# Performance work log

Hardware: AMD Instinct MI355X
Metric: run time of the kernel (lower is better)

Reference implementation:

```python
import jax, jax.numpy as jnp
import numpy as np

B, S = 2, 2048          # 2 sequences of length 2048 (prefill, equal-length varlen batch)
H, HKV, D = 32, 1, 64   # query heads, kv heads (MQA), head size
HID = H * D             # 2048
T = B * S
SCALE = D ** -0.5


def setup_inputs() -> dict:
    key = jax.random.key(0)
    k1, k2, k3 = jax.random.split(key, 3)
    hidden_states = jax.random.normal(k1, (T, HID), dtype=jnp.float32)
    # rotary tables: positions restart per sequence, NeoX half-rotation, base 10000
    inv_freq = 1.0 / (10000.0 ** (jnp.arange(0, D, 2, dtype=jnp.float32) / D))  # [D/2]
    pos = jnp.tile(jnp.arange(S, dtype=jnp.float32), B)                          # [T]
    freqs = pos[:, None] * inv_freq[None, :]                                     # [T, D/2]
    cos = jnp.cos(freqs)[:, None, :]                                             # [T,1,D/2]
    sin = jnp.sin(freqs)[:, None, :]
    w_qkv = jax.random.normal(k2, ((H + 2 * HKV) * D, HID), dtype=jnp.float32) * (HID ** -0.5)
    w_dense = jax.random.normal(k3, (HID, H * D), dtype=jnp.float32) * (HID ** -0.5)
    return {"hidden_states": hidden_states, "cos": cos, "sin": sin,
            "w_qkv": w_qkv, "w_dense": w_dense}


def _rope(x, cos, sin):
    # x: [T, nh, D]; cos/sin: [T, 1, D/2]; NeoX-style half rotation
    x1, x2 = x[..., : D // 2], x[..., D // 2:]
    return jnp.concatenate([x1 * cos - x2 * sin, x2 * cos + x1 * sin], axis=-1)


def reference(hidden_states, cos, sin, w_qkv, w_dense):
    qkv = hidden_states @ w_qkv.T                                # [T, (H+2*HKV)*D]
    q, kvf = jnp.split(qkv, [H * D], axis=1)
    q = q.reshape(T, H, D)
    kv = kvf.reshape(T, 2, HKV, D)
    q = _rope(q, cos, sin)
    k = _rope(kv[:, 0], cos, sin)                                # [T, HKV, D]
    v = kv[:, 1]                                                 # [T, HKV, D]
    # varlen prefill attention: reshape to [B,S,...]; MQA broadcast kv over H heads
    qb = q.reshape(B, S, H, D)
    kb = k.reshape(B, S, HKV, D)[:, :, 0, :]                     # [B,S,D]
    vb = v.reshape(B, S, HKV, D)[:, :, 0, :]
    scores = jnp.einsum("bshd,btd->bhst", qb, kb) * SCALE        # [B,H,S,S]
    causal = jnp.tril(jnp.ones((S, S), dtype=bool))
    scores = jnp.where(causal[None, None], scores, jnp.float32(-1e30))
    probs = jax.nn.softmax(scores, axis=-1)
    attn = jnp.einsum("bhst,btd->bshd", probs, vb)               # [B,S,H,D]
    return attn.reshape(T, H * D) @ w_dense.T                    # [T, HID]
```

## Files before the change

### kernel.cpp

```cpp
#include <hip/hip_runtime.h>

#define BB   2
#define SS   2048
#define TT   4096
#define HH   32
#define DD   64
#define HIDN 2048
#define NQKV 2176
#define QK_SCALE_LOG2 0.1803368801f

#define AS1 __attribute__((address_space(1)))
#define AS3 __attribute__((address_space(3)))

typedef __attribute__((ext_vector_type(8))) short short8;
typedef __attribute__((ext_vector_type(4))) float f32x4;
typedef __attribute__((ext_vector_type(16))) float f32x16;
typedef __attribute__((ext_vector_type(4))) unsigned short ushort4_t;
typedef __attribute__((ext_vector_type(4))) unsigned int uint4_t;

__device__ inline unsigned short f2bf(float f) {
  unsigned int u = __builtin_bit_cast(unsigned int, f);
  u += 0x7FFFu + ((u >> 16) & 1u);
  return (unsigned short)(u >> 16);
}
__device__ inline float bf2f(unsigned short s) {
  unsigned int u = ((unsigned int)s) << 16;
  return __builtin_bit_cast(float, u);
}
__device__ inline float exp2fast(float x) { return __builtin_amdgcn_exp2f(x); }

__global__ __launch_bounds__(256)
void cvt_kernel(const float* __restrict__ in, unsigned short* __restrict__ out, int n4) {
  int i = blockIdx.x * 256 + threadIdx.x;
  if (i >= n4) return;
  float4 v = ((const float4*)in)[i];
  ushort4_t u = { f2bf(v.x), f2bf(v.y), f2bf(v.z), f2bf(v.w) };
  *(ushort4_t*)(out + (long)i * 4) = u;
}

template<int OUT_BF16>
__global__ __launch_bounds__(256)
void gemm_bt(const unsigned short* __restrict__ A, const unsigned short* __restrict__ Bw,
             void* __restrict__ Cp, int M, int N, int K) {
  __shared__ unsigned char lAB[32768];
  const int tid  = threadIdx.x;
  const int lane = tid & 63;
  const int wv   = tid >> 6;
  const int wr   = wv >> 1, wc = wv & 1;
  const int g    = lane >> 4, qq = lane & 15;
  const long bm0 = (long)blockIdx.y * 128;
  const long bn0 = (long)blockIdx.x * 128;
  const int srow  = tid >> 3;
  const int scolu = ((((tid & 7) << 4) ^ ((srow & 7) << 4)) >> 1);

  f32x4 zero = {0.f, 0.f, 0.f, 0.f};
  f32x4 acc[4][4];
#pragma unroll
  for (int m = 0; m < 4; ++m)
#pragma unroll
    for (int n = 0; n < 4; ++n) acc[m][n] = zero;

  const unsigned short* aSrc = A  + (bm0 + srow) * K + scolu;
  const unsigned short* bSrc = Bw + (bn0 + srow) * K + scolu;
  const int rswz = (qq & 7) << 4;

  for (int k0 = 0; k0 < K; k0 += 64) {
    __syncthreads();
#pragma unroll
    for (int gg = 0; gg < 4; ++gg) {
      __builtin_amdgcn_global_load_lds(
          (const AS1 unsigned int*)(aSrc + k0 + (long)32 * gg * K),
          (AS3 unsigned int*)(lAB + gg * 4096 + wv * 1024), 16, 0, 0);
      __builtin_amdgcn_global_load_lds(
          (const AS1 unsigned int*)(bSrc + k0 + (long)32 * gg * K),
          (AS3 unsigned int*)(lAB + 16384 + gg * 4096 + wv * 1024), 16, 0, 0);
    }
    __syncthreads();

#pragma unroll
    for (int ks = 0; ks < 2; ++ks) {
      short8 af[4], bf[4];
#pragma unroll
      for (int m = 0; m < 4; ++m)
        af[m] = *(const short8*)(lAB + (wr * 64 + m * 16 + qq) * 128
                                     + ((ks * 64 + g * 16) ^ rswz));
#pragma unroll
      for (int n = 0; n < 4; ++n)
        bf[n] = *(const short8*)(lAB + 16384 + (wc * 64 + n * 16 + qq) * 128
                                     + ((ks * 64 + g * 16) ^ rswz));
#pragma unroll
      for (int m = 0; m < 4; ++m)
#pragma unroll
        for (int n = 0; n < 4; ++n)
          acc[m][n] = __builtin_amdgcn_mfma_f32_16x16x32_bf16(af[m], bf[n], acc[m][n], 0, 0, 0);
    }
  }

#pragma unroll
  for (int m = 0; m < 4; ++m) {
#pragma unroll
    for (int r = 0; r < 4; ++r) {
      long row = bm0 + wr * 64 + m * 16 + g * 4 + r;
#pragma unroll
      for (int n = 0; n < 4; ++n) {
        long col = bn0 + wc * 64 + n * 16 + qq;
        float v = acc[m][n][r];
        if (OUT_BF16) ((unsigned short*)Cp)[row * N + col] = f2bf(v);
        else          ((float*)Cp)[row * N + col] = v;
      }
    }
  }
}

__global__ __launch_bounds__(256)
void rope_kernel(const unsigned short* __restrict__ qkv, const float* __restrict__ cosb,
                 const float* __restrict__ sinb, unsigned short* __restrict__ q_out,
                 unsigned short* __restrict__ k_out, unsigned short* __restrict__ v_out) {
  int idx = blockIdx.x * 256 + threadIdx.x;
  if (idx >= TT * 136) return;
  int t   = idx / 136;
  int rem = idx - t * 136;
  int hh  = rem >> 2;
  int i0  = (rem & 3) * 8;
  const unsigned short* row = qkv + (long)t * NQKV;

  if (hh < 33) {
    const unsigned short* src = row + (hh < 32 ? hh * 64 : 2048);
    short8 a = *(const short8*)(src + i0);
    short8 b = *(const short8*)(src + 32 + i0);
    float cv[8], sv[8];
    *(float4*)(cv)     = *(const float4*)(cosb + t * 32 + i0);
    *(float4*)(cv + 4) = *(const float4*)(cosb + t * 32 + i0 + 4);
    *(float4*)(sv)     = *(const float4*)(sinb + t * 32 + i0);
    *(float4*)(sv + 4) = *(const float4*)(sinb + t * 32 + i0 + 4);
    const float sc = (hh < 32) ? QK_SCALE_LOG2 : 1.f;
    short8 ra, rb;
#pragma unroll
    for (int j = 0; j < 8; ++j) {
      float x1 = bf2f((unsigned short)a[j]);
      float x2 = bf2f((unsigned short)b[j]);
      ra[j] = (short)f2bf((x1 * cv[j] - x2 * sv[j]) * sc);
      rb[j] = (short)f2bf((x2 * cv[j] + x1 * sv[j]) * sc);
    }
    unsigned short* dst = (hh < 32) ? q_out + ((long)t * 32 + hh) * 64
                                    : k_out + (long)t * 64;
    *(short8*)(dst + i0)      = ra;
    *(short8*)(dst + 32 + i0) = rb;
  } else {
    const unsigned short* src = row + 2112;
    short8 a = *(const short8*)(src + i0);
    short8 b = *(const short8*)(src + 32 + i0);
    int bb = t >> 11, s = t & 2047;
    int tile = s >> 6, c = s & 63;
    long base = ((long)bb * 32 + tile) * 64;
#pragma unroll
    for (int j = 0; j < 8; ++j) {
      v_out[(base + i0 + j) * 64 + c]      = (unsigned short)a[j];
      v_out[(base + 32 + i0 + j) * 64 + c] = (unsigned short)b[j];
    }
  }
}

__global__ __launch_bounds__(256, 2)
void attn_kernel(const unsigned short* __restrict__ qs, const unsigned short* __restrict__ kr,
                 const unsigned short* __restrict__ vt, unsigned short* __restrict__ ob) {
  __shared__ unsigned char lsm[32768];
  const int tid  = threadIdx.x;
  const int lane = tid & 63;
  const int wv   = tid >> 6;
  const int half = lane >> 5;
  const int qc   = lane & 31;
  const int h    = blockIdx.y * 4 + wv;
  const int b    = blockIdx.z;
  const int qtA  = blockIdx.x;
  const int qtB  = (SS / 32 - 1) - blockIdx.x;
  const int q0A  = qtA * 32, q0B = qtB * 32;
  const int nbA  = (q0A >> 7) + 1, nbB = (q0B >> 7) + 1;

  const unsigned short* kb  = kr + (long)b * SS * 64;
  const unsigned short* vtb = vt + (long)b * (SS / 64) * 64 * 64;

  const int srow = tid >> 3;
  const int scol = ((((tid & 7) << 4) ^ ((srow & 7) << 4)) >> 1);

  const int rswz = (qc & 7) << 4;
  int roff[4];
#pragma unroll
  for (int i = 0; i < 4; ++i)
    roff[i] = qc * 128 + ((i * 32 + half * 16) ^ rswz);

  short8 qfA[4], qfB[4];
  {
    const unsigned short* qrA = qs + ((long)(b * SS + q0A + qc) * HH + h) * 64;
    const unsigned short* qrB = qs + ((long)(b * SS + q0B + qc) * HH + h) * 64;
#pragma unroll
    for (int dstep = 0; dstep < 4; ++dstep) {
      qfA[dstep] = *(const short8*)(qrA + dstep * 16 + half * 8);
      qfB[dstep] = *(const short8*)(qrB + dstep * 16 + half * 8);
    }
  }

  f32x16 oA0, oA1, oB0, oB1;
#pragma unroll
  for (int r = 0; r < 16; ++r) { oA0[r] = 0.f; oA1[r] = 0.f; oB0[r] = 0.f; oB1[r] = 0.f; }
  float mA = -1e30f, lA = 0.f, mB = -1e30f, lB = 0.f;

#define PHASE(qf, o0, o1, mst, lst, q0x, isLast)                                 \
  do {                                                                           \
    f32x16 st0, st1;                                                             \
    _Pragma("unroll")                                                            \
    for (int r = 0; r < 16; ++r) { st0[r] = 0.f; st1[r] = 0.f; }                 \
    __builtin_amdgcn_s_setprio(1);                                               \
    _Pragma("unroll")                                                            \
    for (int dstep = 0; dstep < 4; ++dstep) {                                    \
      short8 kfA_ = *(const short8*)(Kb + roff[dstep]);                          \
      short8 kfB_ = *(const short8*)(Kb + roff[dstep] + 4096);                   \
      st0 = __builtin_amdgcn_mfma_f32_32x32x16_bf16(kfA_, qf[dstep], st0, 0, 0, 0); \
      st1 = __builtin_amdgcn_mfma_f32_32x32x16_bf16(kfB_, qf[dstep], st1, 0, 0, 0); \
    }                                                                            \
    __builtin_amdgcn_s_setprio(0);                                               \
    if (isLast) {                                                                \
      _Pragma("unroll")                                                          \
      for (int r = 0; r < 16; ++r) {                                             \
        int rkv = (r & 3) + 8 * (r >> 2) + 4 * half;                             \
        if (kvb + rkv      > (q0x) + qc) st0[r] = -1e30f;                        \
        if (kvb + 32 + rkv > (q0x) + qc) st1[r] = -1e30f;                        \
      }                                                                          \
    }                                                                            \
    float pmax = st0[0];                                                         \
    _Pragma("unroll")                                                            \
    for (int r = 1; r < 16; ++r) pmax = fmaxf(pmax, st0[r]);                     \
    _Pragma("unroll")                                                            \
    for (int r = 0; r < 16; ++r) pmax = fmaxf(pmax, st1[r]);                     \
    pmax = fmaxf(pmax, __shfl_xor(pmax, 32));                                    \
    if (!__all(pmax - mst <= 8.f)) {                                             \
      const float mnew = fmaxf(mst, pmax);                                       \
      const float scal = exp2fast(mst - mnew);                                   \
      lst *= scal;                                                               \
      _Pragma("unroll")                                                          \
      for (int r = 0; r < 16; ++r) { o0[r] *= scal; o1[r] *= scal; }             \
      mst = mnew;                                                                \
    }                                                                            \
    float psum = 0.f;                                                            \
    _Pragma("unroll")                                                            \
    for (int r = 0; r < 16; ++r) { st0[r] = exp2fast(st0[r] - mst); psum += st0[r]; } \
    _Pragma("unroll")                                                            \
    for (int r = 0; r < 16; ++r) { st1[r] = exp2fast(st1[r] - mst); psum += st1[r]; } \
    psum += __shfl_xor(psum, 32);                                                \
    lst += psum;                                                                 \
    short8 pb[4];                                                                \
    _Pragma("unroll")                                                            \
    for (int hseg = 0; hseg < 2; ++hseg) {                                       \
      const f32x16& pp = hseg ? st1 : st0;                                       \
      unsigned int a0, a1, a2, a3, a4, a5, a6, a7;                               \
      asm("v_cvt_pk_bf16_f32 %0, %1, %2" : "=v"(a0) : "v"(pp[0]),  "v"(pp[1]));  \
      asm("v_cvt_pk_bf16_f32 %0, %1, %2" : "=v"(a1) : "v"(pp[2]),  "v"(pp[3]));  \
      asm("v_cvt_pk_bf16_f32 %0, %1, %2" : "=v"(a2) : "v"(pp[4]),  "v"(pp[5]));  \
      asm("v_cvt_pk_bf16_f32 %0, %1, %2" : "=v"(a3) : "v"(pp[6]),  "v"(pp[7]));  \
      asm("v_cvt_pk_bf16_f32 %0, %1, %2" : "=v"(a4) : "v"(pp[8]),  "v"(pp[9]));  \
      asm("v_cvt_pk_bf16_f32 %0, %1, %2" : "=v"(a5) : "v"(pp[10]), "v"(pp[11])); \
      asm("v_cvt_pk_bf16_f32 %0, %1, %2" : "=v"(a6) : "v"(pp[12]), "v"(pp[13])); \
      asm("v_cvt_pk_bf16_f32 %0, %1, %2" : "=v"(a7) : "v"(pp[14]), "v"(pp[15])); \
      asm("v_permlane32_swap_b32 %0, %1" : "+v"(a0), "+v"(a2));                  \
      asm("v_permlane32_swap_b32 %0, %1" : "+v"(a1), "+v"(a3));                  \
      asm("v_permlane32_swap_b32 %0, %1" : "+v"(a4), "+v"(a6));                  \
      asm("v_permlane32_swap_b32 %0, %1" : "+v"(a5), "+v"(a7));                  \
      uint4_t w0 = { a0, a1, a2, a3 };                                           \
      uint4_t w1 = { a4, a5, a6, a7 };                                           \
      pb[hseg * 2]     = __builtin_bit_cast(short8, w0);                         \
      pb[hseg * 2 + 1] = __builtin_bit_cast(short8, w1);                         \
    }                                                                            \
    __builtin_amdgcn_s_setprio(1);                                               \
    _Pragma("unroll")                                                            \
    for (int ks = 0; ks < 4; ++ks) {                                             \
      short8 vfA_ = *(const short8*)(Vb + roff[ks]);                             \
      short8 vfB_ = *(const short8*)(Vb + roff[ks] + 4096);                      \
      o0 = __builtin_amdgcn_mfma_f32_32x32x16_bf16(vfA_, pb[ks], o0, 0, 0, 0);   \
      o1 = __builtin_amdgcn_mfma_f32_32x32x16_bf16(vfB_, pb[ks], o1, 0, 0, 0);   \
    }                                                                            \
    __builtin_amdgcn_s_setprio(0);                                               \
  } while (0)

  for (int ib = 0; ib < nbB; ++ib) {
    const int kv0 = ib * 128;
    __syncthreads();
    {
      const unsigned short* kS = kb + ((long)(kv0 + srow)) * 64 + scol;
#pragma unroll
      for (int gg = 0; gg < 4; ++gg)
        __builtin_amdgcn_global_load_lds((const AS1 unsigned int*)(kS + gg * 32 * 64),
            (AS3 unsigned int*)(lsm + gg * 4096 + wv * 1024), 16, 0, 0);
      const unsigned short* vS = vtb + (long)(2 * ib) * 4096 + srow * 64 + scol;
#pragma unroll
      for (int gg = 0; gg < 4; ++gg)
        __builtin_amdgcn_global_load_lds((const AS1 unsigned int*)(vS + gg * 32 * 64),
            (AS3 unsigned int*)(lsm + 16384 + gg * 4096 + wv * 1024), 16, 0, 0);
    }
    __syncthreads();

    for (int ph = 0; ph < 2; ++ph) {
      const unsigned char* Kb = lsm + ph * 8192;
      const unsigned char* Vb = lsm + 16384 + ph * 8192;
      const int kvb = kv0 + ph * 64;
      if (!(ph && ib == nbB - 1 && (q0B & 127) < 64))
        PHASE(qfB, oB0, oB1, mB, lB, q0B, ib == nbB - 1);
      if (ib < nbA && !(ph && ib == nbA - 1 && (q0A & 127) < 64))
        PHASE(qfA, oA0, oA1, mA, lA, q0A, ib == nbA - 1);
    }
  }
#undef PHASE

  {
    const float inv = 1.f / lA;
    unsigned short* orow = ob + ((long)(b * SS + q0A + qc) * HH + h) * 64;
#pragma unroll
    for (int r = 0; r < 16; ++r) {
      int d0 = (r & 3) + 8 * (r >> 2) + 4 * half;
      orow[d0]      = f2bf(oA0[r] * inv);
      orow[32 + d0] = f2bf(oA1[r] * inv);
    }
  }
  {
    const float inv = 1.f / lB;
    unsigned short* orow = ob + ((long)(b * SS + q0B + qc) * HH + h) * 64;
#pragma unroll
    for (int r = 0; r < 16; ++r) {
      int d0 = (r & 3) + 8 * (r >> 2) + 4 * half;
      orow[d0]      = f2bf(oB0[r] * inv);
      orow[32 + d0] = f2bf(oB1[r] * inv);
    }
  }
}

extern "C" void kernel_launch(void* const* d_in, const int* in_sizes, int n_in,
                              void* d_out, int out_size, void* d_ws, size_t ws_size,
                              hipStream_t stream) {
  const float* hs   = (const float*)d_in[0];
  const float* cosb = (const float*)d_in[1];
  const float* sinb = (const float*)d_in[2];
  const float* wqkv = (const float*)d_in[3];
  const float* wd   = (const float*)d_in[4];

  char* ws = (char*)d_ws;
  unsigned short* hs_bf   = (unsigned short*)(ws);
  unsigned short* wqkv_bf = (unsigned short*)(ws + 16777216);
  unsigned short* wd_bf   = (unsigned short*)(ws + 25690112);
  unsigned short* qkv_bf  = (unsigned short*)(ws + 34078720);
  unsigned short* q_bf    = (unsigned short*)(ws + 51904512);
  unsigned short* k_bf    = (unsigned short*)(ws + 68681728);
  unsigned short* vt_bf   = (unsigned short*)(ws + 69206016);

  cvt_kernel<<<8192, 256, 0, stream>>>(hs,   hs_bf,   2097152);
  cvt_kernel<<<4352, 256, 0, stream>>>(wqkv, wqkv_bf, 1114112);
  cvt_kernel<<<4096, 256, 0, stream>>>(wd,   wd_bf,   1048576);

  gemm_bt<1><<<dim3(17, 32), 256, 0, stream>>>(hs_bf, wqkv_bf, qkv_bf, TT, NQKV, HIDN);

  rope_kernel<<<2176, 256, 0, stream>>>(qkv_bf, cosb, sinb, q_bf, k_bf, vt_bf);

  attn_kernel<<<dim3(SS / 64, 8, BB), 256, 0, stream>>>(q_bf, k_bf, vt_bf, hs_bf);

  gemm_bt<0><<<dim3(16, 32), 256, 0, stream>>>(hs_bf, wd_bf, d_out, TT, HIDN, HIDN);
}
```

Measured before the change: 184.3 us.

## Fuse RoPE and QKV split into QKV GEMM epilogue; merge conversion kernels

The QKV projection GEMM now applies rotary embedding and the Q scale directly in its epilogue, writing Q, K and transposed V straight to their attention layouts. This removes the intermediate bf16 qkv buffer and the separate rope kernel. The three fp32-to-bf16 conversion launches are merged into one launch over a contiguous workspace. The cost is scattered 2-byte stores in the epilogue, including strided transposed V writes and per-element cos/sin loads, which coalesce poorly.

```diff
diff --git a/kernel.cpp b/kernel.cpp
--- a/kernel.cpp
+++ b/kernel.cpp
@@ -30,18 +30,22 @@
 __device__ inline float exp2fast(float x) { return __builtin_amdgcn_exp2f(x); }
 
 __global__ __launch_bounds__(256)
-void cvt_kernel(const float* __restrict__ in, unsigned short* __restrict__ out, int n4) {
+void cvt_all_kernel(const float* __restrict__ hs, const float* __restrict__ wqkv,
+                    const float* __restrict__ wd, unsigned short* __restrict__ out) {
   int i = blockIdx.x * 256 + threadIdx.x;
-  if (i >= n4) return;
-  float4 v = ((const float4*)in)[i];
+  if (i >= 4259840) return;
+  const float* src; int off;
+  if (i < 2097152)      { src = hs;   off = i; }
+  else if (i < 3211264) { src = wqkv; off = i - 2097152; }
+  else                  { src = wd;   off = i - 3211264; }
+  float4 v = ((const float4*)src)[off];
   ushort4_t u = { f2bf(v.x), f2bf(v.y), f2bf(v.z), f2bf(v.w) };
   *(ushort4_t*)(out + (long)i * 4) = u;
 }
 
-template<int OUT_BF16>
 __global__ __launch_bounds__(256)
-void gemm_bt(const unsigned short* __restrict__ A, const unsigned short* __restrict__ Bw,
-             void* __restrict__ Cp, int M, int N, int K) {
+void gemm_dense(const unsigned short* __restrict__ A, const unsigned short* __restrict__ Bw,
+                float* __restrict__ Cp, int M, int N, int K) {
   __shared__ unsigned char lAB[32768];
   const int tid  = threadIdx.x;
   const int lane = tid & 63;
@@ -102,61 +106,123 @@
     for (int r = 0; r < 4; ++r) {
       long row = bm0 + wr * 64 + m * 16 + g * 4 + r;
 #pragma unroll
-      for (int n = 0; n < 4; ++n) {
-        long col = bn0 + wc * 64 + n * 16 + qq;
-        float v = acc[m][n][r];
-        if (OUT_BF16) ((unsigned short*)Cp)[row * N + col] = f2bf(v);
-        else          ((float*)Cp)[row * N + col] = v;
+      for (int n = 0; n < 4; ++n)
+        Cp[row * N + bn0 + wc * 64 + n * 16 + qq] = acc[m][n][r];
+    }
+  }
+}
+
+__global__ __launch_bounds__(256)
+void gemm_qkv(const unsigned short* __restrict__ A, const unsigned short* __restrict__ Bw,
+              const float* __restrict__ cosb, const float* __restrict__ sinb,
+              unsigned short* __restrict__ q_out, unsigned short* __restrict__ k_out,
+              unsigned short* __restrict__ v_out) {
+  __shared__ unsigned char lAB[32768];
+  const int K = HIDN, N = NQKV;
+  const int tid  = threadIdx.x;
+  const int lane = tid & 63;
+  const int wv   = tid >> 6;
+  const int wr   = wv >> 1, wc = wv & 1;
+  const int g    = lane >> 4, qq = lane & 15;
+  const long bm0 = (long)blockIdx.y * 128;
+  const long bn0 = (long)blockIdx.x * 128;
+  const int srow  = tid >> 3;
+  const int scolu = ((((tid & 7) << 4) ^ ((srow & 7) << 4)) >> 1);
+
+  f32x4 zero = {0.f, 0.f, 0.f, 0.f};
+  f32x4 acc[4][4];
+#pragma unroll
+  for (int m = 0; m < 4; ++m)
+#pragma unroll
+    for (int n = 0; n < 4; ++n) acc[m][n] = zero;
+
+  const unsigned short* aSrc = A  + (bm0 + srow) * K + scolu;
+  const unsigned short* bSrc = Bw + (bn0 + srow) * K + scolu;
+  const int rswz = (qq & 7) << 4;
+
+  for (int k0 = 0; k0 < K; k0 += 64) {
+    __syncthreads();
+#pragma unroll
+    for (int gg = 0; gg < 4; ++gg) {
+      __builtin_amdgcn_global_load_lds(
+          (const AS1 unsigned int*)(aSrc + k0 + (long)32 * gg * K),
+          (AS3 unsigned int*)(lAB + gg * 4096 + wv * 1024), 16, 0, 0);
+      __builtin_amdgcn_global_load_lds(
+          (const AS1 unsigned int*)(bSrc + k0 + (long)32 * gg * K),
+          (AS3 unsigned int*)(lAB + 16384 + gg * 4096 + wv * 1024), 16, 0, 0);
+    }
+    __syncthreads();
+
+#pragma unroll
+    for (int ks = 0; ks < 2; ++ks) {
+      short8 af[4], bf[4];
+#pragma unroll
+      for (int m = 0; m < 4; ++m)
+        af[m] = *(const short8*)(lAB + (wr * 64 + m * 16 + qq) * 128
+                                     + ((ks * 64 + g * 16) ^ rswz));
+#pragma unroll
+      for (int n = 0; n < 4; ++n)
+        bf[n] = *(const short8*)(lAB + 16384 + (wc * 64 + n * 16 + qq) * 128
+                                     + ((ks * 64 + g * 16) ^ rswz));
+#pragma unroll
+      for (int m = 0; m < 4; ++m)
+#pragma unroll
+        for (int n = 0; n < 4; ++n)
+          acc[m][n] = __builtin_amdgcn_mfma_f32_16x16x32_bf16(af[m], bf[n], acc[m][n], 0, 0, 0);
+    }
+  }
+
+  const int colbase = (int)bn0 + wc * 64;
+  if (colbase < 2048) {
+    const int head = colbase >> 6;
+#pragma unroll
+    for (int m = 0; m < 4; ++m) {
+#pragma unroll
+      for (int r = 0; r < 4; ++r) {
+        long t = bm0 + wr * 64 + m * 16 + g * 4 + r;
+        unsigned short* qr = q_out + ((long)t * 32 + head) * 64;
+#pragma unroll
+        for (int n = 0; n < 2; ++n) {
+          int i = n * 16 + qq;
+          float cv = cosb[t * 32 + i], sv = sinb[t * 32 + i];
+          float x1 = acc[m][n][r], x2 = acc[m][n + 2][r];
+          qr[i]      = f2bf((x1 * cv - x2 * sv) * QK_SCALE_LOG2);
+          qr[32 + i] = f2bf((x2 * cv + x1 * sv) * QK_SCALE_LOG2);
+        }
       }
     }
-  }
-}
-
-__global__ __launch_bounds__(256)
-void rope_kernel(const unsigned short* __restrict__ qkv, const float* __restrict__ cosb,
-                 const float* __restrict__ sinb, unsigned short* __restrict__ q_out,
-                 unsigned short* __restrict__ k_out, unsigned short* __restrict__ v_out) {
-  int idx = blockIdx.x * 256 + threadIdx.x;
-  if (idx >= TT * 136) return;
-  int t   = idx / 136;
-  int rem = idx - t * 136;
-  int hh  = rem >> 2;
-  int i0  = (rem & 3) * 8;
-  const unsigned short* row = qkv + (long)t * NQKV;
-
-  if (hh < 33) {
-    const unsigned short* src = row + (hh < 32 ? hh * 64 : 2048);
-    short8 a = *(const short8*)(src + i0);
-    short8 b = *(const short8*)(src + 32 + i0);
-    float cv[8], sv[8];
-    *(float4*)(cv)     = *(const float4*)(cosb + t * 32 + i0);
-    *(float4*)(cv + 4) = *(const float4*)(cosb + t * 32 + i0 + 4);
-    *(float4*)(sv)     = *(const float4*)(sinb + t * 32 + i0);
-    *(float4*)(sv + 4) = *(const float4*)(sinb + t * 32 + i0 + 4);
-    const float sc = (hh < 32) ? QK_SCALE_LOG2 : 1.f;
-    short8 ra, rb;
-#pragma unroll
-    for (int j = 0; j < 8; ++j) {
-      float x1 = bf2f((unsigned short)a[j]);
-      float x2 = bf2f((unsigned short)b[j]);
-      ra[j] = (short)f2bf((x1 * cv[j] - x2 * sv[j]) * sc);
-      rb[j] = (short)f2bf((x2 * cv[j] + x1 * sv[j]) * sc);
-    }
-    unsigned short* dst = (hh < 32) ? q_out + ((long)t * 32 + hh) * 64
-                                    : k_out + (long)t * 64;
-    *(short8*)(dst + i0)      = ra;
-    *(short8*)(dst + 32 + i0) = rb;
+  } else if (colbase < 2112) {
+#pragma unroll
+    for (int m = 0; m < 4; ++m) {
+#pragma unroll
+      for (int r = 0; r < 4; ++r) {
+        long t = bm0 + wr * 64 + m * 16 + g * 4 + r;
+        unsigned short* kr2 = k_out + (long)t * 64;
+#pragma unroll
+        for (int n = 0; n < 2; ++n) {
+          int i = n * 16 + qq;
+          float cv = cosb[t * 32 + i], sv = sinb[t * 32 + i];
+          float x1 = acc[m][n][r], x2 = acc[m][n + 2][r];
+          kr2[i]      = f2bf(x1 * cv - x2 * sv);
+          kr2[32 + i] = f2bf(x2 * cv + x1 * sv);
+        }
+      }
+    }
   } else {
-    const unsigned short* src = row + 2112;
-    short8 a = *(const short8*)(src + i0);
-    short8 b = *(const short8*)(src + 32 + i0);
-    int bb = t >> 11, s = t & 2047;
-    int tile = s >> 6, c = s & 63;
-    long base = ((long)bb * 32 + tile) * 64;
-#pragma unroll
-    for (int j = 0; j < 8; ++j) {
-      v_out[(base + i0 + j) * 64 + c]      = (unsigned short)a[j];
-      v_out[(base + 32 + i0 + j) * 64 + c] = (unsigned short)b[j];
+#pragma unroll
+    for (int m = 0; m < 4; ++m) {
+#pragma unroll
+      for (int r = 0; r < 4; ++r) {
+        long t   = bm0 + wr * 64 + m * 16 + g * 4 + r;
+        int  bb  = (int)(t >> 11), s = (int)(t & 2047);
+        long base = ((long)bb * 32 + (s >> 6)) * 64;
+        int  c    = s & 63;
+#pragma unroll
+        for (int n = 0; n < 4; ++n) {
+          int d = n * 16 + qq;
+          v_out[(base + d) * 64 + c] = f2bf(acc[m][n][r]);
+        }
+      }
     }
   }
 }
@@ -345,20 +411,17 @@
   unsigned short* hs_bf   = (unsigned short*)(ws);
   unsigned short* wqkv_bf = (unsigned short*)(ws + 16777216);
   unsigned short* wd_bf   = (unsigned short*)(ws + 25690112);
-  unsigned short* qkv_bf  = (unsigned short*)(ws + 34078720);
   unsigned short* q_bf    = (unsigned short*)(ws + 51904512);
   unsigned short* k_bf    = (unsigned short*)(ws + 68681728);
   unsigned short* vt_bf   = (unsigned short*)(ws + 69206016);
 
-  cvt_kernel<<<8192, 256, 0, stream>>>(hs,   hs_bf,   2097152);
-  cvt_kernel<<<4352, 256, 0, stream>>>(wqkv, wqkv_bf, 1114112);
-  cvt_kernel<<<4096, 256, 0, stream>>>(wd,   wd_bf,   1048576);
-
-  gemm_bt<1><<<dim3(17, 32), 256, 0, stream>>>(hs_bf, wqkv_bf, qkv_bf, TT, NQKV, HIDN);
-
-  rope_kernel<<<2176, 256, 0, stream>>>(qkv_bf, cosb, sinb, q_bf, k_bf, vt_bf);
+  cvt_all_kernel<<<16640, 256, 0, stream>>>(hs, wqkv, wd, hs_bf);
+
+  gemm_qkv<<<dim3(17, 32), 256, 0, stream>>>(hs_bf, wqkv_bf, cosb, sinb,
+                                             q_bf, k_bf, vt_bf);
 
   attn_kernel<<<dim3(SS / 64, 8, BB), 256, 0, stream>>>(q_bf, k_bf, vt_bf, hs_bf);
 
-  gemm_bt<0><<<dim3(16, 32), 256, 0, stream>>>(hs_bf, wd_bf, d_out, TT, HIDN, HIDN);
-}
+  gemm_dense<<<dim3(16, 32), 256, 0, stream>>>(hs_bf, wd_bf, (float*)d_out,
+                                               TT, HIDN, HIDN);
+}
```

Measured after the change: 189.8 us. +3.0%, slower.
